# Optimization experiments

Hardware: AMD Instinct MI355X
Metric: run time of the kernel (lower is better)

## Reference

```python
import jax, jax.numpy as jnp
import numpy as np

N = 100000
E = 1600000
BN_EPS = 1e-5


def setup_inputs() -> dict:
    key = jax.random.key(0)
    ks = jax.random.split(key, 12)
    d = 128
    s = 1.0 / np.sqrt(d)
    inp = {
        "x": jax.random.normal(ks[0], (N, d), jnp.float32),
        "x_importance": jax.random.uniform(ks[1], (N, 1), jnp.float32),
        "edge_index": jax.random.randint(ks[2], (2, E), 0, N, jnp.int64),
        "bn_gamma": jnp.ones((d,), jnp.float32),
        "bn_beta": jnp.zeros((d,), jnp.float32),
        "Wfc": jax.random.normal(ks[3], (d, d), jnp.float32) * s,
    }
    for i in range(1, 6):
        inp[f"W{i}"] = jax.random.normal(ks[3 + i], (d, d), jnp.float32) * s
        inp[f"b{i}"] = jnp.zeros((d,), jnp.float32)
    return inp


def reference(x, x_importance, edge_index, bn_gamma, bn_beta,
              W1, b1, W2, b2, W3, b3, W4, b4, W5, b5, Wfc):
    src, dst = edge_index[0], edge_index[1]

    # bn_in (training-mode batch stats over nodes)
    h = x * x_importance
    mean = jnp.mean(h, axis=0)
    var = jnp.mean(jnp.square(h - mean), axis=0)  # biased, as torch BN normalize
    h = (h - mean) * jax.lax.rsqrt(var + BN_EPS) * bn_gamma + bn_beta

    def gin_conv(h, W, b):
        # GINConv with eps=0: nn(h + sum_{j in N(i)} h_j)
        agg = jax.ops.segment_sum(h[src], dst, num_segments=N)  # [N, d]
        return jnp.tanh((h + agg) @ W + b)

    xs = []
    for W, b in ((W1, b1), (W2, b2), (W3, b3), (W4, b4), (W5, b5)):
        h = gin_conv(h, W, b)
        xs.append(h)
    xs.append(jnp.tanh(h @ Wfc))
    return jnp.concatenate(xs, axis=-1)  # [N, 5*dim + out_channels]
```

## Files before the change

### kernel.cpp

```cpp
#include <hip/hip_runtime.h>
#include <hip/hip_fp16.h>
#include <cstdint>
#include <cstddef>

#define DIM 128
#define BN_EPS_ 1e-5f

typedef _Float16 half8 __attribute__((ext_vector_type(8)));
typedef float floatx4 __attribute__((ext_vector_type(4)));
typedef short shortx8 __attribute__((ext_vector_type(8)));

#define SCALE_H 32768.f
#define INV_H   (1.f/32768.f)

__device__ __forceinline__ float fast_tanh(float x) {
    float t = __expf(2.f * x);
    return 1.f - 2.f / (t + 1.f);
}

__device__ __forceinline__ short quant(float v, float scale) {
    int q = __float2int_rn(v * scale);
    q = max(min(q, 32767), -32767);
    return (short)q;
}

__global__ __launch_bounds__(256) void k_stats(
    const float* __restrict__ x, const float* __restrict__ imp,
    float* __restrict__ gsum, float* __restrict__ gsq, float* __restrict__ gmax, int N)
{
    __shared__ float ls[256], lq[256], lm[256];
    int t = threadIdx.x;
    int f = t & 127;
    int rs = t >> 7;
    float s = 0.f, q = 0.f, m = 0.f;
    for (int r = blockIdx.x * 2 + rs; r < N; r += gridDim.x * 2) {
        float v = x[(size_t)r * DIM + f] * imp[r];
        s += v; q += v * v; m = fmaxf(m, fabsf(v));
    }
    ls[t] = s; lq[t] = q; lm[t] = m;
    __syncthreads();
    if (t < 128) {
        atomicAdd(&gsum[f], ls[t] + ls[t + 128]);
        atomicAdd(&gsq[f],  lq[t] + lq[t + 128]);
        float mm = fmaxf(lm[t], lm[t + 128]);
        atomicMax((int*)&gmax[f], __float_as_int(mm));
    }
}

__global__ void k_finalize(const float* __restrict__ gsum, const float* __restrict__ gsq,
                           const float* __restrict__ gmax,
                           const float* __restrict__ gamma, const float* __restrict__ beta,
                           float* __restrict__ scale, float* __restrict__ shift,
                           float* __restrict__ q0, int N)
{
    __shared__ float sb[128];
    int f = threadIdx.x;
    float mean = gsum[f] / (float)N;
    float var  = gsq[f] / (float)N - mean * mean;
    var = fmaxf(var, 0.f);
    float sc = gamma[f] * rsqrtf(var + BN_EPS_);
    float sh = beta[f] - mean * sc;
    scale[f] = sc;
    shift[f] = sh;
    sb[f] = fabsf(sc) * gmax[f] + fabsf(sh);
    __syncthreads();
    for (int off = 64; off > 0; off >>= 1) {
        if (f < off) sb[f] = fmaxf(sb[f], sb[f + off]);
        __syncthreads();
    }
    if (f == 0) {
        float Q = fmaxf(sb[0], 1e-20f);
        q0[0] = 32766.f / Q;
        q0[1] = Q / 32766.f;
    }
}

__global__ __launch_bounds__(256) void k_bn_quant(
    const float* __restrict__ x, const float* __restrict__ imp,
    const float* __restrict__ scale, const float* __restrict__ shift,
    const float* __restrict__ q0, short* __restrict__ hq0, int n32)
{
    int i = blockIdx.x * 256 + threadIdx.x;
    if (i >= n32) return;
    float qs = q0[0];
    int r = i >> 5, f4 = i & 31;
    float im = imp[r];
    float4 v  = ((const float4*)x)[i];
    float4 sc = ((const float4*)scale)[f4];
    float4 sh = ((const float4*)shift)[f4];
    short q[4];
    q[0] = quant(fmaf(v.x * im, sc.x, sh.x), qs);
    q[1] = quant(fmaf(v.y * im, sc.y, sh.y), qs);
    q[2] = quant(fmaf(v.z * im, sc.z, sh.z), qs);
    q[3] = quant(fmaf(v.w * im, sc.w, sh.w), qs);
    *(float2*)(hq0 + (size_t)i * 4) = *(float2*)q;
}

__global__ __launch_bounds__(256) void k_wsplit(const float* __restrict__ W,
                                               _Float16* __restrict__ WtHi,
                                               _Float16* __restrict__ WtLo)
{
    for (int e = blockIdx.x * 256 + threadIdx.x; e < DIM * DIM; e += gridDim.x * 256) {
        int k = e >> 7, n = e & 127;
        float w = W[e];
        _Float16 hi = (_Float16)w;
        _Float16 lo = (_Float16)(w - (float)hi);
        WtHi[n * DIM + k] = hi;
        WtLo[n * DIM + k] = lo;
    }
}

__global__ void k_hist(const int* __restrict__ dst, int* __restrict__ deg, int E)
{
    int e = blockIdx.x * 256 + threadIdx.x;
    if (e < E) atomicAdd(&deg[dst[e]], 1);
}

__global__ __launch_bounds__(256) void k_chunksum(const int* __restrict__ deg, int* __restrict__ csum, int N)
{
    __shared__ int s[256];
    int t = threadIdx.x;
    int i = blockIdx.x * 256 + t;
    s[t] = (i < N) ? deg[i] : 0;
    __syncthreads();
    for (int off = 128; off > 0; off >>= 1) {
        if (t < off) s[t] += s[t + off];
        __syncthreads();
    }
    if (t == 0) csum[blockIdx.x] = s[0];
}

__global__ void k_scanchunks(int* __restrict__ csum, int* __restrict__ rstart, int nchunks, int N)
{
    __shared__ int s[512];
    int t = threadIdx.x;
    s[t] = (t < nchunks) ? csum[t] : 0;
    __syncthreads();
    for (int off = 1; off < 512; off <<= 1) {
        int add = (t >= off) ? s[t - off] : 0;
        __syncthreads();
        s[t] += add;
        __syncthreads();
    }
    if (t < nchunks) csum[t] = (t > 0) ? s[t - 1] : 0;
    if (t == 511) rstart[N] = s[511];
}

__global__ __launch_bounds__(256) void k_scanwithin(
    const int* __restrict__ deg, const int* __restrict__ csum,
    int* __restrict__ rstart, int* __restrict__ cursor, int N)
{
    __shared__ int s[256];
    int t = threadIdx.x;
    int i = blockIdx.x * 256 + t;
    int v = (i < N) ? deg[i] : 0;
    s[t] = v;
    __syncthreads();
    for (int off = 1; off < 256; off <<= 1) {
        int add = (t >= off) ? s[t - off] : 0;
        __syncthreads();
        s[t] += add;
        __syncthreads();
    }
    if (i < N) {
        int rs = csum[blockIdx.x] + s[t] - v;
        rstart[i] = rs;
        cursor[i] = rs;
    }
}

__global__ void k_scatter(const int* __restrict__ src, const int* __restrict__ dst,
                          int* __restrict__ cursor, int* __restrict__ csr, int E)
{
    int e = blockIdx.x * 256 + threadIdx.x;
    if (e < E) {
        int d = dst[e];
        int pos = atomicAdd(&cursor[d], 1);
        csr[pos] = src[e];
    }
}

template<int FINAL>
__global__ __launch_bounds__(128) void k_layer(
    const short* __restrict__ hqIn,
    const int* __restrict__ rstart, const int* __restrict__ csr,
    const float* __restrict__ invPtr, float invConst,
    const _Float16* __restrict__ WtHi, const _Float16* __restrict__ WtLo,
    const float* __restrict__ bias,
    const _Float16* __restrict__ WfHi, const _Float16* __restrict__ WfLo,
    float* __restrict__ outS,
    float* __restrict__ outF,
    short* __restrict__ hqOut,
    int N)
{
    __shared__ float sA[32][132];
    int t = threadIdx.x;
    float inv = invPtr ? invPtr[0] : invConst;

    {
        int l16 = t & 15;
        int sg  = t >> 4;
        const shortx8* base = (const shortx8*)hqIn;
#pragma unroll
        for (int pass = 0; pass < 4; ++pass) {
            int nl = pass * 8 + sg;
            int node = blockIdx.x * 32 + nl;
            float* dstp = &sA[nl][l16 * 8];
            if (node < N) {
                int beg = rstart[node], end = rstart[node + 1];
                shortx8 sv = base[(size_t)node * 16 + l16];
                int acc[8];
#pragma unroll
                for (int j = 0; j < 8; ++j) acc[j] = (int)sv[j];
                int e = beg;
                if (e + 4 <= end) {
                    shortx8 b0 = base[(size_t)csr[e]     * 16 + l16];
                    shortx8 b1 = base[(size_t)csr[e + 1] * 16 + l16];
                    shortx8 b2 = base[(size_t)csr[e + 2] * 16 + l16];
                    shortx8 b3 = base[(size_t)csr[e + 3] * 16 + l16];
                    e += 4;
                    for (; e + 4 <= end; e += 4) {
                        shortx8 c0 = base[(size_t)csr[e]     * 16 + l16];
                        shortx8 c1 = base[(size_t)csr[e + 1] * 16 + l16];
                        shortx8 c2 = base[(size_t)csr[e + 2] * 16 + l16];
                        shortx8 c3 = base[(size_t)csr[e + 3] * 16 + l16];
#pragma unroll
                        for (int j = 0; j < 8; ++j)
                            acc[j] += ((int)b0[j] + (int)b1[j]) + ((int)b2[j] + (int)b3[j]);
                        b0 = c0; b1 = c1; b2 = c2; b3 = c3;
                    }
#pragma unroll
                    for (int j = 0; j < 8; ++j)
                        acc[j] += ((int)b0[j] + (int)b1[j]) + ((int)b2[j] + (int)b3[j]);
                }
                for (; e < end; ++e) {
                    shortx8 v0 = base[(size_t)csr[e] * 16 + l16];
#pragma unroll
                    for (int j = 0; j < 8; ++j) acc[j] += (int)v0[j];
                }
#pragma unroll
                for (int j = 0; j < 8; ++j) dstp[j] = acc[j] * inv;
            } else {
#pragma unroll
                for (int j = 0; j < 8; ++j) dstp[j] = 0.f;
            }
        }
    }
    __syncthreads();

    int wave = t >> 6;
    int lane = t & 63;
    int kg = (lane >> 4) * 8;
    int arowL = wave * 16 + (lane & 15);

    half8 ahi[4], alo[4];
#pragma unroll
    for (int ks = 0; ks < 4; ++ks) {
        float4 f0 = *(const float4*)&sA[arowL][ks * 32 + kg];
        float4 f1 = *(const float4*)&sA[arowL][ks * 32 + kg + 4];
        float fv[8] = {f0.x, f0.y, f0.z, f0.w, f1.x, f1.y, f1.z, f1.w};
#pragma unroll
        for (int j = 0; j < 8; ++j) {
            _Float16 h = (_Float16)fv[j];
            ahi[ks][j] = h;
            alo[ks][j] = (_Float16)(fv[j] - (float)h);
        }
    }

    floatx4 acc[8];
#pragma unroll
    for (int nt = 0; nt < 8; ++nt) acc[nt] = (floatx4){0.f, 0.f, 0.f, 0.f};
#pragma unroll
    for (int nt = 0; nt < 8; ++nt) {
        int ncol = nt * 16 + (lane & 15);
#pragma unroll
        for (int ks = 0; ks < 4; ++ks) {
            half8 bhi = *(const half8*)(WtHi + (size_t)ncol * DIM + ks * 32 + kg);
            half8 blo = *(const half8*)(WtLo + (size_t)ncol * DIM + ks * 32 + kg);
            acc[nt] = __builtin_amdgcn_mfma_f32_16x16x32_f16(ahi[ks], bhi, acc[nt], 0, 0, 0);
            acc[nt] = __builtin_amdgcn_mfma_f32_16x16x32_f16(alo[ks], bhi, acc[nt], 0, 0, 0);
            acc[nt] = __builtin_amdgcn_mfma_f32_16x16x32_f16(ahi[ks], blo, acc[nt], 0, 0, 0);
        }
    }

    int rbaseL = wave * 16 + (lane >> 4) * 4;
    int rglob = blockIdx.x * 32 + rbaseL;
    float tv[8][4];
#pragma unroll
    for (int nt = 0; nt < 8; ++nt) {
        int col = nt * 16 + (lane & 15);
        float bv = bias[col];
#pragma unroll
        for (int j = 0; j < 4; ++j) {
            float tt = fast_tanh(acc[nt][j] + bv);
            tv[nt][j] = tt;
            int r = rglob + j;
            if (r < N) {
                outS[(size_t)r * 768 + col] = tt;
                if (hqOut) hqOut[(size_t)r * DIM + col] = quant(tt, SCALE_H);
            }
        }
    }

    if (FINAL) {
        __syncthreads();
#pragma unroll
        for (int nt = 0; nt < 8; ++nt) {
            int col = nt * 16 + (lane & 15);
#pragma unroll
            for (int j = 0; j < 4; ++j)
                sA[rbaseL + j][col] = tv[nt][j];
        }
        __syncthreads();

        half8 chi[4], clo[4];
#pragma unroll
        for (int ks = 0; ks < 4; ++ks) {
            float4 f0 = *(const float4*)&sA[arowL][ks * 32 + kg];
            float4 f1 = *(const float4*)&sA[arowL][ks * 32 + kg + 4];
            float fv[8] = {f0.x, f0.y, f0.z, f0.w, f1.x, f1.y, f1.z, f1.w};
#pragma unroll
            for (int j = 0; j < 8; ++j) {
                _Float16 h = (_Float16)fv[j];
                chi[ks][j] = h;
                clo[ks][j] = (_Float16)(fv[j] - (float)h);
            }
        }
        floatx4 ac2[8];
#pragma unroll
        for (int nt = 0; nt < 8; ++nt) ac2[nt] = (floatx4){0.f, 0.f, 0.f, 0.f};
#pragma unroll
        for (int nt = 0; nt < 8; ++nt) {
            int ncol = nt * 16 + (lane & 15);
#pragma unroll
            for (int ks = 0; ks < 4; ++ks) {
                half8 bhi = *(const half8*)(WfHi + (size_t)ncol * DIM + ks * 32 + kg);
                half8 blo = *(const half8*)(WfLo + (size_t)ncol * DIM + ks * 32 + kg);
                ac2[nt] = __builtin_amdgcn_mfma_f32_16x16x32_f16(chi[ks], bhi, ac2[nt], 0, 0, 0);
                ac2[nt] = __builtin_amdgcn_mfma_f32_16x16x32_f16(clo[ks], bhi, ac2[nt], 0, 0, 0);
                ac2[nt] = __builtin_amdgcn_mfma_f32_16x16x32_f16(chi[ks], blo, ac2[nt], 0, 0, 0);
            }
        }
#pragma unroll
        for (int nt = 0; nt < 8; ++nt) {
            int col = nt * 16 + (lane & 15);
#pragma unroll
            for (int j = 0; j < 4; ++j) {
                int r = rglob + j;
                if (r < N) outF[(size_t)r * 768 + col] = fast_tanh(ac2[nt][j]);
            }
        }
    }
}

extern "C" void kernel_launch(void* const* d_in, const int* in_sizes, int n_in,
                              void* d_out, int out_size, void* d_ws, size_t ws_size,
                              hipStream_t stream)
{
    const float* x     = (const float*)d_in[0];
    const float* imp   = (const float*)d_in[1];
    const int*   eidx  = (const int*)d_in[2];
    const float* gamma = (const float*)d_in[3];
    const float* beta  = (const float*)d_in[4];
    const float* Wfc   = (const float*)d_in[5];
    const float* W[5]; const float* B[5];
    for (int i = 0; i < 5; ++i) {
        W[i] = (const float*)d_in[6 + 2 * i];
        B[i] = (const float*)d_in[7 + 2 * i];
    }
    float* out = (float*)d_out;

    const int N = in_sizes[0] / DIM;
    const int E = in_sizes[2] / 2;
    const int* src = eidx;
    const int* dst = eidx + E;

    char* ws = (char*)d_ws;
    size_t off = 0;
    auto alloc = [&](size_t b) -> char* {
        char* p = ws + off;
        off = (off + b + 255) & ~(size_t)255;
        return p;
    };
    short* hqA = (short*)alloc((size_t)N * DIM * 2);
    short* hqB = (short*)alloc((size_t)N * DIM * 2);
    _Float16* WtHi[6]; _Float16* WtLo[6];
    for (int i = 0; i < 6; ++i) {
        WtHi[i] = (_Float16*)alloc(DIM * DIM * 2);
        WtLo[i] = (_Float16*)alloc(DIM * DIM * 2);
    }
    int*   deg    = (int*)alloc((size_t)N * 4);
    int*   rstart = (int*)alloc((size_t)(N + 1) * 4);
    int*   cursor = (int*)alloc((size_t)N * 4);
    int*   csr    = (int*)alloc((size_t)E * 4);
    float* gsum   = (float*)alloc(128 * 4);
    float* gsq    = (float*)alloc(128 * 4);
    float* gmax   = (float*)alloc(128 * 4);
    float* scale  = (float*)alloc(128 * 4);
    float* shift  = (float*)alloc(128 * 4);
    float* q0     = (float*)alloc(2 * 4);
    int*   csum   = (int*)alloc(4096 * 4);

    hipMemsetAsync(gsum, 0, 128 * 4, stream);
    hipMemsetAsync(gsq,  0, 128 * 4, stream);
    hipMemsetAsync(gmax, 0, 128 * 4, stream);
    hipMemsetAsync(deg,  0, (size_t)N * 4, stream);

    k_stats<<<1024, 256, 0, stream>>>(x, imp, gsum, gsq, gmax, N);
    k_finalize<<<1, 128, 0, stream>>>(gsum, gsq, gmax, gamma, beta, scale, shift, q0, N);
    k_bn_quant<<<(N * 32 + 255) / 256, 256, 0, stream>>>(x, imp, scale, shift, q0, hqA, N * 32);

    k_hist<<<(E + 255) / 256, 256, 0, stream>>>(dst, deg, E);
    int nchunks = (N + 255) / 256;
    k_chunksum<<<nchunks, 256, 0, stream>>>(deg, csum, N);
    k_scanchunks<<<1, 512, 0, stream>>>(csum, rstart, nchunks, N);
    k_scanwithin<<<nchunks, 256, 0, stream>>>(deg, csum, rstart, cursor, N);
    k_scatter<<<(E + 255) / 256, 256, 0, stream>>>(src, dst, cursor, csr, E);

    for (int i = 0; i < 5; ++i)
        k_wsplit<<<8, 256, 0, stream>>>(W[i], WtHi[i], WtLo[i]);
    k_wsplit<<<8, 256, 0, stream>>>(Wfc, WtHi[5], WtLo[5]);

    int grid = (N + 31) / 32;
    short* cur = hqA;
    short* nxt = hqB;
    for (int l = 0; l < 4; ++l) {
        k_layer<0><<<grid, 128, 0, stream>>>(cur, rstart, csr,
            (l == 0) ? (q0 + 1) : nullptr, INV_H,
            WtHi[l], WtLo[l], B[l], nullptr, nullptr,
            out + (size_t)l * DIM, nullptr, nxt, N);
        short* tmp = cur; cur = nxt; nxt = tmp;
    }
    k_layer<1><<<grid, 128, 0, stream>>>(cur, rstart, csr,
        nullptr, INV_H,
        WtHi[4], WtLo[4], B[4], WtHi[5], WtLo[5],
        out + (size_t)4 * DIM, out + (size_t)5 * DIM, nullptr, N);
}
```

Before: 993.9 us.

## Aggregate neighbors with one wave per node using scalar CSR indices

The gather-aggregation phase changes from 16 lanes per node handling 8 shorts each to a whole wave per node, with each lane loading 4 bytes. Row offsets and neighbor indices are made wave-uniform with readfirstlane so they can go through scalar loads. The inner loop now keeps 8 neighbors in flight instead of 4. The aim is to cut per-lane index loads and raise memory-level parallelism, but each wave now walks 16 nodes one after another and each lane issues narrower loads, which adds more serial latency.

```diff
diff --git a/kernel.cpp b/kernel.cpp
--- a/kernel.cpp
+++ b/kernel.cpp
@@ -8,7 +8,6 @@
 
 typedef _Float16 half8 __attribute__((ext_vector_type(8)));
 typedef float floatx4 __attribute__((ext_vector_type(4)));
-typedef short shortx8 __attribute__((ext_vector_type(8)));
 
 #define SCALE_H 32768.f
 #define INV_H   (1.f/32768.f)
@@ -196,62 +195,94 @@
     __shared__ float sA[32][132];
     int t = threadIdx.x;
     float inv = invPtr ? invPtr[0] : invConst;
-
-    {
-        int l16 = t & 15;
-        int sg  = t >> 4;
-        const shortx8* base = (const shortx8*)hqIn;
-#pragma unroll
-        for (int pass = 0; pass < 4; ++pass) {
-            int nl = pass * 8 + sg;
-            int node = blockIdx.x * 32 + nl;
-            float* dstp = &sA[nl][l16 * 8];
-            if (node < N) {
-                int beg = rstart[node], end = rstart[node + 1];
-                shortx8 sv = base[(size_t)node * 16 + l16];
-                int acc[8];
-#pragma unroll
-                for (int j = 0; j < 8; ++j) acc[j] = (int)sv[j];
-                int e = beg;
-                if (e + 4 <= end) {
-                    shortx8 b0 = base[(size_t)csr[e]     * 16 + l16];
-                    shortx8 b1 = base[(size_t)csr[e + 1] * 16 + l16];
-                    shortx8 b2 = base[(size_t)csr[e + 2] * 16 + l16];
-                    shortx8 b3 = base[(size_t)csr[e + 3] * 16 + l16];
-                    e += 4;
-                    for (; e + 4 <= end; e += 4) {
-                        shortx8 c0 = base[(size_t)csr[e]     * 16 + l16];
-                        shortx8 c1 = base[(size_t)csr[e + 1] * 16 + l16];
-                        shortx8 c2 = base[(size_t)csr[e + 2] * 16 + l16];
-                        shortx8 c3 = base[(size_t)csr[e + 3] * 16 + l16];
-#pragma unroll
-                        for (int j = 0; j < 8; ++j)
-                            acc[j] += ((int)b0[j] + (int)b1[j]) + ((int)b2[j] + (int)b3[j]);
-                        b0 = c0; b1 = c1; b2 = c2; b3 = c3;
-                    }
-#pragma unroll
-                    for (int j = 0; j < 8; ++j)
-                        acc[j] += ((int)b0[j] + (int)b1[j]) + ((int)b2[j] + (int)b3[j]);
+    int lane = t & 63;
+    int wv = __builtin_amdgcn_readfirstlane(t >> 6);
+
+    const unsigned* __restrict__ hw = (const unsigned*)hqIn;
+
+    for (int i = 0; i < 16; ++i) {
+        int nl = wv * 16 + i;
+        int node = blockIdx.x * 32 + nl;
+        int acc0 = 0, acc1 = 0;
+        if (node < N) {
+            int beg = __builtin_amdgcn_readfirstlane(rstart[node]);
+            int end = __builtin_amdgcn_readfirstlane(rstart[node + 1]);
+            unsigned sv = hw[(size_t)node * 64 + lane];
+            acc0 = (int)(short)(sv & 0xffffu);
+            acc1 = (int)(short)(sv >> 16);
+            int e = beg;
+            if (e + 8 <= end) {
+                unsigned b0, b1, b2, b3, b4, b5, b6, b7;
+                {
+                    unsigned i0 = (unsigned)__builtin_amdgcn_readfirstlane(csr[e]);
+                    unsigned i1 = (unsigned)__builtin_amdgcn_readfirstlane(csr[e + 1]);
+                    unsigned i2 = (unsigned)__builtin_amdgcn_readfirstlane(csr[e + 2]);
+                    unsigned i3 = (unsigned)__builtin_amdgcn_readfirstlane(csr[e + 3]);
+                    unsigned i4 = (unsigned)__builtin_amdgcn_readfirstlane(csr[e + 4]);
+                    unsigned i5 = (unsigned)__builtin_amdgcn_readfirstlane(csr[e + 5]);
+                    unsigned i6 = (unsigned)__builtin_amdgcn_readfirstlane(csr[e + 6]);
+                    unsigned i7 = (unsigned)__builtin_amdgcn_readfirstlane(csr[e + 7]);
+                    b0 = hw[(size_t)i0 * 64 + lane];
+                    b1 = hw[(size_t)i1 * 64 + lane];
+                    b2 = hw[(size_t)i2 * 64 + lane];
+                    b3 = hw[(size_t)i3 * 64 + lane];
+                    b4 = hw[(size_t)i4 * 64 + lane];
+                    b5 = hw[(size_t)i5 * 64 + lane];
+                    b6 = hw[(size_t)i6 * 64 + lane];
+                    b7 = hw[(size_t)i7 * 64 + lane];
                 }
-                for (; e < end; ++e) {
-                    shortx8 v0 = base[(size_t)csr[e] * 16 + l16];
-#pragma unroll
-                    for (int j = 0; j < 8; ++j) acc[j] += (int)v0[j];
+                e += 8;
+                for (; e + 8 <= end; e += 8) {
+                    unsigned i0 = (unsigned)__builtin_amdgcn_readfirstlane(csr[e]);
+                    unsigned i1 = (unsigned)__builtin_amdgcn_readfirstlane(csr[e + 1]);
+                    unsigned i2 = (unsigned)__builtin_amdgcn_readfirstlane(csr[e + 2]);
+                    unsigned i3 = (unsigned)__builtin_amdgcn_readfirstlane(csr[e + 3]);
+                    unsigned i4 = (unsigned)__builtin_amdgcn_readfirstlane(csr[e + 4]);
+                    unsigned i5 = (unsigned)__builtin_amdgcn_readfirstlane(csr[e + 5]);
+                    unsigned i6 = (unsigned)__builtin_amdgcn_readfirstlane(csr[e + 6]);
+                    unsigned i7 = (unsigned)__builtin_amdgcn_readfirstlane(csr[e + 7]);
+                    unsigned c0 = hw[(size_t)i0 * 64 + lane];
+                    unsigned c1 = hw[(size_t)i1 * 64 + lane];
+                    unsigned c2 = hw[(size_t)i2 * 64 + lane];
+                    unsigned c3 = hw[(size_t)i3 * 64 + lane];
+                    unsigned c4 = hw[(size_t)i4 * 64 + lane];
+                    unsigned c5 = hw[(size_t)i5 * 64 + lane];
+                    unsigned c6 = hw[(size_t)i6 * 64 + lane];
+                    unsigned c7 = hw[(size_t)i7 * 64 + lane];
+                    acc0 += (int)(short)(b0 & 0xffffu) + (int)(short)(b1 & 0xffffu)
+                          + (int)(short)(b2 & 0xffffu) + (int)(short)(b3 & 0xffffu)
+                          + (int)(short)(b4 & 0xffffu) + (int)(short)(b5 & 0xffffu)
+                          + (int)(short)(b6 & 0xffffu) + (int)(short)(b7 & 0xffffu);
+                    acc1 += (int)(short)(b0 >> 16) + (int)(short)(b1 >> 16)
+                          + (int)(short)(b2 >> 16) + (int)(short)(b3 >> 16)
+                          + (int)(short)(b4 >> 16) + (int)(short)(b5 >> 16)
+                          + (int)(short)(b6 >> 16) + (int)(short)(b7 >> 16);
+                    b0 = c0; b1 = c1; b2 = c2; b3 = c3;
+                    b4 = c4; b5 = c5; b6 = c6; b7 = c7;
                 }
-#pragma unroll
-                for (int j = 0; j < 8; ++j) dstp[j] = acc[j] * inv;
-            } else {
-#pragma unroll
-                for (int j = 0; j < 8; ++j) dstp[j] = 0.f;
-            }
-        }
-    }
-    __syncthreads();
-
-    int wave = t >> 6;
-    int lane = t & 63;
+                acc0 += (int)(short)(b0 & 0xffffu) + (int)(short)(b1 & 0xffffu)
+                      + (int)(short)(b2 & 0xffffu) + (int)(short)(b3 & 0xffffu)
+                      + (int)(short)(b4 & 0xffffu) + (int)(short)(b5 & 0xffffu)
+                      + (int)(short)(b6 & 0xffffu) + (int)(short)(b7 & 0xffffu);
+                acc1 += (int)(short)(b0 >> 16) + (int)(short)(b1 >> 16)
+                      + (int)(short)(b2 >> 16) + (int)(short)(b3 >> 16)
+                      + (int)(short)(b4 >> 16) + (int)(short)(b5 >> 16)
+                      + (int)(short)(b6 >> 16) + (int)(short)(b7 >> 16);
+            }
+            for (; e < end; ++e) {
+                unsigned i0 = (unsigned)__builtin_amdgcn_readfirstlane(csr[e]);
+                unsigned v = hw[(size_t)i0 * 64 + lane];
+                acc0 += (int)(short)(v & 0xffffu);
+                acc1 += (int)(short)(v >> 16);
+            }
+        }
+        sA[nl][lane * 2]     = acc0 * inv;
+        sA[nl][lane * 2 + 1] = acc1 * inv;
+    }
+    __syncthreads();
+
     int kg = (lane >> 4) * 8;
-    int arowL = wave * 16 + (lane & 15);
+    int arowL = wv * 16 + (lane & 15);
 
     half8 ahi[4], alo[4];
 #pragma unroll
@@ -283,7 +314,7 @@
         }
     }
 
-    int rbaseL = wave * 16 + (lane >> 4) * 4;
+    int rbaseL = wv * 16 + (lane >> 4) * 4;
     int rglob = blockIdx.x * 32 + rbaseL;
     float tv[8][4];
 #pragma unroll
```

New measurement: 1.127 ms. 13.4% more time.

## Bucket CSR neighbors by source chunk and stage block edge indices in LDS

Applied to the files above, without the earlier changes.

Builds a two-level CSR in which each destination's neighbors are grouped into source-node chunks of 8192. The layer kernel iterates chunk by chunk across all 32 nodes of a block, so concurrent gathers hit a narrower range of source rows and get better L2 locality. Neighbor indices for each block are also preloaded into shared memory. This adds extra preprocessing kernels (a per-node, per-chunk histogram, a scan and a scatter) plus N*NC-sized buffers, and shortens the gather unroll from 4 to 2, which may reduce memory-level parallelism.

```diff
diff --git a/kernel.cpp b/kernel.cpp
--- a/kernel.cpp
+++ b/kernel.cpp
@@ -5,6 +5,8 @@
 
 #define DIM 128
 #define BN_EPS_ 1e-5f
+#define CH_SHIFT 13
+#define MAXNC1 17
 
 typedef _Float16 half8 __attribute__((ext_vector_type(8)));
 typedef float floatx4 __attribute__((ext_vector_type(4)));
@@ -148,7 +150,7 @@
 
 __global__ __launch_bounds__(256) void k_scanwithin(
     const int* __restrict__ deg, const int* __restrict__ csum,
-    int* __restrict__ rstart, int* __restrict__ cursor, int N)
+    int* __restrict__ rstart, int N)
 {
     __shared__ int s[256];
     int t = threadIdx.x;
@@ -162,28 +164,47 @@
         s[t] += add;
         __syncthreads();
     }
-    if (i < N) {
-        int rs = csum[blockIdx.x] + s[t] - v;
-        rstart[i] = rs;
-        cursor[i] = rs;
-    }
-}
-
-__global__ void k_scatter(const int* __restrict__ src, const int* __restrict__ dst,
-                          int* __restrict__ cursor, int* __restrict__ csr, int E)
+    if (i < N) rstart[i] = csum[blockIdx.x] + s[t] - v;
+}
+
+__global__ void k_hist13(const int* __restrict__ src, const int* __restrict__ dst,
+                         int* __restrict__ cnt13, int NC, int E)
+{
+    int e = blockIdx.x * 256 + threadIdx.x;
+    if (e < E) atomicAdd(&cnt13[dst[e] * NC + (src[e] >> CH_SHIFT)], 1);
+}
+
+__global__ void k_rs2(const int* __restrict__ rstart, const int* __restrict__ cnt13,
+                      int* __restrict__ rs2, int* __restrict__ cursor13, int NC, int N)
+{
+    int n = blockIdx.x * 256 + threadIdx.x;
+    if (n >= N) return;
+    int run = rstart[n];
+    rs2[n * (NC + 1)] = run;
+    for (int c = 0; c < NC; ++c) {
+        int cc = cnt13[n * NC + c];
+        cursor13[n * NC + c] = run;
+        run += cc;
+        rs2[n * (NC + 1) + c + 1] = run;
+    }
+}
+
+__global__ void k_scatter13(const int* __restrict__ src, const int* __restrict__ dst,
+                            int* __restrict__ cursor13, int* __restrict__ csr, int NC, int E)
 {
     int e = blockIdx.x * 256 + threadIdx.x;
     if (e < E) {
-        int d = dst[e];
-        int pos = atomicAdd(&cursor[d], 1);
-        csr[pos] = src[e];
+        int s = src[e];
+        int pos = atomicAdd(&cursor13[dst[e] * NC + (s >> CH_SHIFT)], 1);
+        csr[pos] = s;
     }
 }
 
 template<int FINAL>
 __global__ __launch_bounds__(128) void k_layer(
     const short* __restrict__ hqIn,
-    const int* __restrict__ rstart, const int* __restrict__ csr,
+    const int* __restrict__ rstart, const int* __restrict__ rs2,
+    const int* __restrict__ csr, int NC,
     const float* __restrict__ invPtr, float invConst,
     const _Float16* __restrict__ WtHi, const _Float16* __restrict__ WtLo,
     const float* __restrict__ bias,
@@ -193,57 +214,82 @@
     short* __restrict__ hqOut,
     int N)
 {
+    constexpr int CAP = 1536;
     __shared__ float sA[32][132];
+    __shared__ int sIdx[CAP];
+    __shared__ int sRs[32 * MAXNC1];
     int t = threadIdx.x;
     float inv = invPtr ? invPtr[0] : invConst;
+    int NC1 = NC + 1;
+
+    int node0 = blockIdx.x * 32;
+    int nLocal = (node0 + 32 <= N) ? 32 : (N - node0);
+    int bbeg = __builtin_amdgcn_readfirstlane(rstart[node0]);
+    int bend = __builtin_amdgcn_readfirstlane(rstart[node0 + nLocal]);
+    int L = bend - bbeg;
+    int Ls = L < CAP ? L : CAP;
+    for (int i = t; i < Ls; i += 128) sIdx[i] = csr[bbeg + i];
+    {
+        int tot = nLocal * NC1;
+        const int* r2 = rs2 + (size_t)node0 * NC1;
+        for (int i = t; i < 32 * NC1; i += 128)
+            sRs[i] = (i < tot) ? (r2[i] - bbeg) : 0;
+    }
+    __syncthreads();
 
     {
         int l16 = t & 15;
         int sg  = t >> 4;
         const shortx8* base = (const shortx8*)hqIn;
+
+        auto fetch = [&](int e) -> unsigned {
+            return (unsigned)((e < CAP) ? sIdx[e] : csr[bbeg + e]);
+        };
+
+        int acc[4][8];
+#pragma unroll
+        for (int pass = 0; pass < 4; ++pass) {
+            int node = node0 + pass * 8 + sg;
+            if (node < N) {
+                shortx8 sv = base[(size_t)node * 16 + l16];
+#pragma unroll
+                for (int j = 0; j < 8; ++j) acc[pass][j] = (int)sv[j];
+            } else {
+#pragma unroll
+                for (int j = 0; j < 8; ++j) acc[pass][j] = 0;
+            }
+        }
+
+        for (int c = 0; c < NC; ++c) {
+#pragma unroll
+            for (int pass = 0; pass < 4; ++pass) {
+                int nl = pass * 8 + sg;
+                int e0 = sRs[nl * NC1 + c];
+                int e1 = sRs[nl * NC1 + c + 1];
+                int e = e0;
+                for (; e + 2 <= e1; e += 2) {
+                    unsigned u0 = fetch(e), u1 = fetch(e + 1);
+                    shortx8 r0 = base[(size_t)u0 * 16 + l16];
+                    shortx8 r1 = base[(size_t)u1 * 16 + l16];
+#pragma unroll
+                    for (int j = 0; j < 8; ++j)
+                        acc[pass][j] += (int)r0[j] + (int)r1[j];
+                }
+                if (e < e1) {
+                    unsigned u0 = fetch(e);
+                    shortx8 r0 = base[(size_t)u0 * 16 + l16];
+#pragma unroll
+                    for (int j = 0; j < 8; ++j) acc[pass][j] += (int)r0[j];
+                }
+            }
+        }
+
 #pragma unroll
         for (int pass = 0; pass < 4; ++pass) {
             int nl = pass * 8 + sg;
-            int node = blockIdx.x * 32 + nl;
             float* dstp = &sA[nl][l16 * 8];
-            if (node < N) {
-                int beg = rstart[node], end = rstart[node + 1];
-                shortx8 sv = base[(size_t)node * 16 + l16];
-                int acc[8];
-#pragma unroll
-                for (int j = 0; j < 8; ++j) acc[j] = (int)sv[j];
-                int e = beg;
-                if (e + 4 <= end) {
-                    shortx8 b0 = base[(size_t)csr[e]     * 16 + l16];
-                    shortx8 b1 = base[(size_t)csr[e + 1] * 16 + l16];
-                    shortx8 b2 = base[(size_t)csr[e + 2] * 16 + l16];
-                    shortx8 b3 = base[(size_t)csr[e + 3] * 16 + l16];
-                    e += 4;
-                    for (; e + 4 <= end; e += 4) {
-                        shortx8 c0 = base[(size_t)csr[e]     * 16 + l16];
-                        shortx8 c1 = base[(size_t)csr[e + 1] * 16 + l16];
-                        shortx8 c2 = base[(size_t)csr[e + 2] * 16 + l16];
-                        shortx8 c3 = base[(size_t)csr[e + 3] * 16 + l16];
-#pragma unroll
-                        for (int j = 0; j < 8; ++j)
-                            acc[j] += ((int)b0[j] + (int)b1[j]) + ((int)b2[j] + (int)b3[j]);
-                        b0 = c0; b1 = c1; b2 = c2; b3 = c3;
-                    }
-#pragma unroll
-                    for (int j = 0; j < 8; ++j)
-                        acc[j] += ((int)b0[j] + (int)b1[j]) + ((int)b2[j] + (int)b3[j]);
-                }
-                for (; e < end; ++e) {
-                    shortx8 v0 = base[(size_t)csr[e] * 16 + l16];
-#pragma unroll
-                    for (int j = 0; j < 8; ++j) acc[j] += (int)v0[j];
-                }
-#pragma unroll
-                for (int j = 0; j < 8; ++j) dstp[j] = acc[j] * inv;
-            } else {
-#pragma unroll
-                for (int j = 0; j < 8; ++j) dstp[j] = 0.f;
-            }
+#pragma unroll
+            for (int j = 0; j < 8; ++j) dstp[j] = acc[pass][j] * inv;
         }
     }
     __syncthreads();
@@ -374,6 +420,7 @@
     const int E = in_sizes[2] / 2;
     const int* src = eidx;
     const int* dst = eidx + E;
+    const int NC = ((N - 1) >> CH_SHIFT) + 1;
 
     char* ws = (char*)d_ws;
     size_t off = 0;
@@ -389,22 +436,25 @@
         WtHi[i] = (_Float16*)alloc(DIM * DIM * 2);
         WtLo[i] = (_Float16*)alloc(DIM * DIM * 2);
     }
-    int*   deg    = (int*)alloc((size_t)N * 4);
-    int*   rstart = (int*)alloc((size_t)(N + 1) * 4);
-    int*   cursor = (int*)alloc((size_t)N * 4);
-    int*   csr    = (int*)alloc((size_t)E * 4);
-    float* gsum   = (float*)alloc(128 * 4);
-    float* gsq    = (float*)alloc(128 * 4);
-    float* gmax   = (float*)alloc(128 * 4);
-    float* scale  = (float*)alloc(128 * 4);
-    float* shift  = (float*)alloc(128 * 4);
-    float* q0     = (float*)alloc(2 * 4);
-    int*   csum   = (int*)alloc(4096 * 4);
-
-    hipMemsetAsync(gsum, 0, 128 * 4, stream);
-    hipMemsetAsync(gsq,  0, 128 * 4, stream);
-    hipMemsetAsync(gmax, 0, 128 * 4, stream);
-    hipMemsetAsync(deg,  0, (size_t)N * 4, stream);
+    int*   deg      = (int*)alloc((size_t)N * 4);
+    int*   rstart   = (int*)alloc((size_t)(N + 1) * 4);
+    int*   csr      = (int*)alloc((size_t)E * 4);
+    int*   cnt13    = (int*)alloc((size_t)N * NC * 4);
+    int*   rs2      = (int*)alloc((size_t)N * (NC + 1) * 4);
+    int*   cursor13 = (int*)alloc((size_t)N * NC * 4);
+    float* gsum     = (float*)alloc(128 * 4);
+    float* gsq      = (float*)alloc(128 * 4);
+    float* gmax     = (float*)alloc(128 * 4);
+    float* scale    = (float*)alloc(128 * 4);
+    float* shift    = (float*)alloc(128 * 4);
+    float* q0       = (float*)alloc(2 * 4);
+    int*   csum     = (int*)alloc(4096 * 4);
+
+    hipMemsetAsync(gsum,  0, 128 * 4, stream);
+    hipMemsetAsync(gsq,   0, 128 * 4, stream);
+    hipMemsetAsync(gmax,  0, 128 * 4, stream);
+    hipMemsetAsync(deg,   0, (size_t)N * 4, stream);
+    hipMemsetAsync(cnt13, 0, (size_t)N * NC * 4, stream);
 
     k_stats<<<1024, 256, 0, stream>>>(x, imp, gsum, gsq, gmax, N);
     k_finalize<<<1, 128, 0, stream>>>(gsum, gsq, gmax, gamma, beta, scale, shift, q0, N);
@@ -414,8 +464,10 @@
     int nchunks = (N + 255) / 256;
     k_chunksum<<<nchunks, 256, 0, stream>>>(deg, csum, N);
     k_scanchunks<<<1, 512, 0, stream>>>(csum, rstart, nchunks, N);
-    k_scanwithin<<<nchunks, 256, 0, stream>>>(deg, csum, rstart, cursor, N);
-    k_scatter<<<(E + 255) / 256, 256, 0, stream>>>(src, dst, cursor, csr, E);
+    k_scanwithin<<<nchunks, 256, 0, stream>>>(deg, csum, rstart, N);
+    k_hist13<<<(E + 255) / 256, 256, 0, stream>>>(src, dst, cnt13, NC, E);
+    k_rs2<<<(N + 255) / 256, 256, 0, stream>>>(rstart, cnt13, rs2, cursor13, NC, N);
+    k_scatter13<<<(E + 255) / 256, 256, 0, stream>>>(src, dst, cursor13, csr, NC, E);
 
     for (int i = 0; i < 5; ++i)
         k_wsplit<<<8, 256, 0, stream>>>(W[i], WtHi[i], WtLo[i]);
@@ -425,13 +477,13 @@
     short* cur = hqA;
     short* nxt = hqB;
     for (int l = 0; l < 4; ++l) {
-        k_layer<0><<<grid, 128, 0, stream>>>(cur, rstart, csr,
+        k_layer<0><<<grid, 128, 0, stream>>>(cur, rstart, rs2, csr, NC,
             (l == 0) ? (q0 + 1) : nullptr, INV_H,
             WtHi[l], WtLo[l], B[l], nullptr, nullptr,
             out + (size_t)l * DIM, nullptr, nxt, N);
         short* tmp = cur; cur = nxt; nxt = tmp;
     }
-    k_layer<1><<<grid, 128, 0, stream>>>(cur, rstart, csr,
+    k_layer<1><<<grid, 128, 0, stream>>>(cur, rstart, rs2, csr, NC,
         nullptr, INV_H,
         WtHi[4], WtLo[4], B[4], WtHi[5], WtLo[5],
         out + (size_t)4 * DIM, out + (size_t)5 * DIM, nullptr, N);
```

Result: slower. 1.486 ms (+49.5%).

## Halve rows per block and split output columns across waves; nontemporal output stores

Applied to the files above, without the earlier changes.

Each layer block now handles 16 nodes instead of 32, and the two waves split the 128 output columns rather than the rows. This doubles the grid and gives more parallelism for the gather phase. The trade-off is that each block re-reads the full weight matrix for half as many rows, and the MFMA work per wave halves. Output stores to the large concatenated result now use nontemporal hints to avoid polluting the cache.

```diff
diff --git a/kernel.cpp b/kernel.cpp
--- a/kernel.cpp
+++ b/kernel.cpp
@@ -193,18 +193,19 @@
     short* __restrict__ hqOut,
     int N)
 {
-    __shared__ float sA[32][132];
+    __shared__ float sA[16][132];
     int t = threadIdx.x;
     float inv = invPtr ? invPtr[0] : invConst;
+    int node0 = blockIdx.x * 16;
 
     {
         int l16 = t & 15;
         int sg  = t >> 4;
         const shortx8* base = (const shortx8*)hqIn;
 #pragma unroll
-        for (int pass = 0; pass < 4; ++pass) {
+        for (int pass = 0; pass < 2; ++pass) {
             int nl = pass * 8 + sg;
-            int node = blockIdx.x * 32 + nl;
+            int node = node0 + nl;
             float* dstp = &sA[nl][l16 * 8];
             if (node < N) {
                 int beg = rstart[node], end = rstart[node + 1];
@@ -250,14 +251,15 @@
 
     int wave = t >> 6;
     int lane = t & 63;
+    int colbase = wave * 64;
     int kg = (lane >> 4) * 8;
-    int arowL = wave * 16 + (lane & 15);
+    int arow = lane & 15;
 
     half8 ahi[4], alo[4];
 #pragma unroll
     for (int ks = 0; ks < 4; ++ks) {
-        float4 f0 = *(const float4*)&sA[arowL][ks * 32 + kg];
-        float4 f1 = *(const float4*)&sA[arowL][ks * 32 + kg + 4];
+        float4 f0 = *(const float4*)&sA[arow][ks * 32 + kg];
+        float4 f1 = *(const float4*)&sA[arow][ks * 32 + kg + 4];
         float fv[8] = {f0.x, f0.y, f0.z, f0.w, f1.x, f1.y, f1.z, f1.w};
 #pragma unroll
         for (int j = 0; j < 8; ++j) {
@@ -267,12 +269,12 @@
         }
     }
 
-    floatx4 acc[8];
-#pragma unroll
-    for (int nt = 0; nt < 8; ++nt) acc[nt] = (floatx4){0.f, 0.f, 0.f, 0.f};
-#pragma unroll
-    for (int nt = 0; nt < 8; ++nt) {
-        int ncol = nt * 16 + (lane & 15);
+    floatx4 acc[4];
+#pragma unroll
+    for (int nt = 0; nt < 4; ++nt) acc[nt] = (floatx4){0.f, 0.f, 0.f, 0.f};
+#pragma unroll
+    for (int nt = 0; nt < 4; ++nt) {
+        int ncol = colbase + nt * 16 + (lane & 15);
 #pragma unroll
         for (int ks = 0; ks < 4; ++ks) {
             half8 bhi = *(const half8*)(WtHi + (size_t)ncol * DIM + ks * 32 + kg);
@@ -283,20 +285,19 @@
         }
     }
 
-    int rbaseL = wave * 16 + (lane >> 4) * 4;
-    int rglob = blockIdx.x * 32 + rbaseL;
-    float tv[8][4];
-#pragma unroll
-    for (int nt = 0; nt < 8; ++nt) {
-        int col = nt * 16 + (lane & 15);
+    int rbase = (lane >> 4) * 4;
+    float tv[4][4];
+#pragma unroll
+    for (int nt = 0; nt < 4; ++nt) {
+        int col = colbase + nt * 16 + (lane & 15);
         float bv = bias[col];
 #pragma unroll
         for (int j = 0; j < 4; ++j) {
             float tt = fast_tanh(acc[nt][j] + bv);
             tv[nt][j] = tt;
-            int r = rglob + j;
+            int r = node0 + rbase + j;
             if (r < N) {
-                outS[(size_t)r * 768 + col] = tt;
+                __builtin_nontemporal_store(tt, &outS[(size_t)r * 768 + col]);
                 if (hqOut) hqOut[(size_t)r * DIM + col] = quant(tt, SCALE_H);
             }
         }
@@ -305,19 +306,19 @@
     if (FINAL) {
         __syncthreads();
 #pragma unroll
-        for (int nt = 0; nt < 8; ++nt) {
-            int col = nt * 16 + (lane & 15);
+        for (int nt = 0; nt < 4; ++nt) {
+            int col = colbase + nt * 16 + (lane & 15);
 #pragma unroll
             for (int j = 0; j < 4; ++j)
-                sA[rbaseL + j][col] = tv[nt][j];
+                sA[rbase + j][col] = tv[nt][j];
         }
         __syncthreads();
 
         half8 chi[4], clo[4];
 #pragma unroll
         for (int ks = 0; ks < 4; ++ks) {
-            float4 f0 = *(const float4*)&sA[arowL][ks * 32 + kg];
-            float4 f1 = *(const float4*)&sA[arowL][ks * 32 + kg + 4];
+            float4 f0 = *(const float4*)&sA[arow][ks * 32 + kg];
+            float4 f1 = *(const float4*)&sA[arow][ks * 32 + kg + 4];
             float fv[8] = {f0.x, f0.y, f0.z, f0.w, f1.x, f1.y, f1.z, f1.w};
 #pragma unroll
             for (int j = 0; j < 8; ++j) {
@@ -326,12 +327,12 @@
                 clo[ks][j] = (_Float16)(fv[j] - (float)h);
             }
         }
-        floatx4 ac2[8];
-#pragma unroll
-        for (int nt = 0; nt < 8; ++nt) ac2[nt] = (floatx4){0.f, 0.f, 0.f, 0.f};
-#pragma unroll
-        for (int nt = 0; nt < 8; ++nt) {
-            int ncol = nt * 16 + (lane & 15);
+        floatx4 ac2[4];
+#pragma unroll
+        for (int nt = 0; nt < 4; ++nt) ac2[nt] = (floatx4){0.f, 0.f, 0.f, 0.f};
+#pragma unroll
+        for (int nt = 0; nt < 4; ++nt) {
+            int ncol = colbase + nt * 16 + (lane & 15);
 #pragma unroll
             for (int ks = 0; ks < 4; ++ks) {
                 half8 bhi = *(const half8*)(WfHi + (size_t)ncol * DIM + ks * 32 + kg);
@@ -342,12 +343,13 @@
             }
         }
 #pragma unroll
-        for (int nt = 0; nt < 8; ++nt) {
-            int col = nt * 16 + (lane & 15);
+        for (int nt = 0; nt < 4; ++nt) {
+            int col = colbase + nt * 16 + (lane & 15);
 #pragma unroll
             for (int j = 0; j < 4; ++j) {
-                int r = rglob + j;
-                if (r < N) outF[(size_t)r * 768 + col] = fast_tanh(ac2[nt][j]);
+                int r = node0 + rbase + j;
+                if (r < N)
+                    __builtin_nontemporal_store(fast_tanh(ac2[nt][j]), &outF[(size_t)r * 768 + col]);
             }
         }
     }
@@ -421,7 +423,7 @@
         k_wsplit<<<8, 256, 0, stream>>>(W[i], WtHi[i], WtLo[i]);
     k_wsplit<<<8, 256, 0, stream>>>(Wfc, WtHi[5], WtLo[5]);
 
-    int grid = (N + 31) / 32;
+    int grid = (N + 15) / 16;
     short* cur = hqA;
     short* nxt = hqB;
     for (int l = 0; l < 4; ++l) {
```

New measurement: 941.2 us. -5.3%, faster.
